# Kernel tuning notes

Measured on AMD Instinct MI355X. Metric: run time of the kernel, lower is better.

## Reference

```python
import jax, jax.numpy as jnp
import numpy as np

THRESHOLD = 1.25
CURRENT_DECAY = 0.25
VOLTAGE_DECAY = 0.03
SPIKE_PROB = 0.2


def setup_inputs() -> dict:
    key = jax.random.key(0)
    k1, k2 = jax.random.split(key)
    B, N, T = 2048, 16, 1024
    # binary input spike trains [batch, neurons, time]
    spike = (jax.random.uniform(k1, (B, N, T)) < SPIKE_PROB).astype(jnp.float32)
    # Dense synapse weight [out, in], no bias (lava-dl Dense default)
    W = jax.random.normal(k2, (N, N), dtype=jnp.float32) / np.sqrt(N)
    return {"spike": spike, "W": W}


def _cuba_dense(spike, W):
    # synaptic current input per timestep: z[b,o,t]
    z = jnp.einsum('oi,bit->bot', W, spike)
    zt = jnp.moveaxis(z, -1, 0)  # [T, B, O] for scan over time

    def step(carry, x):
        c, v = carry
        c = c * (1.0 - CURRENT_DECAY) + x
        v = v * (1.0 - VOLTAGE_DECAY) + c
        s = (v >= THRESHOLD).astype(v.dtype)
        v = v * (1.0 - s)  # hard reset to zero on spike
        return (c, v), s

    zero = jnp.zeros_like(zt[0])
    _, s = jax.lax.scan(step, (zero, zero), zt)  # s: [T, B, O]
    return jnp.moveaxis(s, 0, -1)  # [B, O, T]


def reference(spike, W):
    y = _cuba_dense(spike, W)  # [B, O, T] binary spikes
    # log-cosh free energy: exp(sum_neurons log(2 cosh(y))) -> [B, T]
    return jnp.exp(jnp.sum(jnp.log(2.0 * jnp.cosh(y)), axis=1))
```

## Files before the change

### kernel.cpp

```cpp
#include <hip/hip_runtime.h>
#include <stdint.h>

#define T_STEPS 1024
#define NWORDS  256
#define NB      8
#define SCAN_BLOCK (NB * 16)

typedef float f32x4 __attribute__((ext_vector_type(4)));

__global__ __launch_bounds__(256) void k_maskify(const float* __restrict__ spike,
                                                 unsigned long long* __restrict__ masks) {
    const int b  = blockIdx.x;
    const int tc = threadIdx.x;
    const float4* sp = reinterpret_cast<const float4*>(spike) + (size_t)b * (16 * NWORDS);
    unsigned int m0 = 0, m1 = 0, m2 = 0, m3 = 0;
#pragma unroll
    for (int i = 0; i < 16; ++i) {
        float4 v = sp[i * NWORDS + tc];
        m0 |= (v.x >= 0.5f) ? (1u << i) : 0u;
        m1 |= (v.y >= 0.5f) ? (1u << i) : 0u;
        m2 |= (v.z >= 0.5f) ? (1u << i) : 0u;
        m3 |= (v.w >= 0.5f) ? (1u << i) : 0u;
    }
    masks[(size_t)b * NWORDS + tc] =
        (unsigned long long)m0 | ((unsigned long long)m1 << 16) |
        ((unsigned long long)m2 << 32) | ((unsigned long long)m3 << 48);
}

__global__ __launch_bounds__(SCAN_BLOCK, 1) void k_scan(const float* __restrict__ W,
                                                        const unsigned long long* __restrict__ masks,
                                                        float* __restrict__ out) {
    __shared__ double ztab8[2][256][17];
    __shared__ unsigned long long mlds[NB][NWORDS + 1];

    const int tid = threadIdx.x;
    const int bb  = tid >> 4;
    const int o   = tid & 15;
    const int b   = blockIdx.x * NB + bb;

    {
        double w[16];
#pragma unroll
        for (int j = 0; j < 16; ++j) w[j] = (double)W[o * 16 + j];
#pragma unroll
        for (int k = 0; k < 64; ++k) {
            const int e    = tid + k * SCAN_BLOCK;
            const int byte = (e >> 4) & 255;
            const int s    = k >> 5;
            double slo = 0.0, shi = 0.0;
#pragma unroll
            for (int j = 0; j < 4; ++j) slo += (byte & (1 << j))  ? w[8 * s + j]     : 0.0;
#pragma unroll
            for (int j = 0; j < 4; ++j) shi += (byte & (16 << j)) ? w[8 * s + 4 + j] : 0.0;
            ztab8[s][byte][o] = slo + shi;
        }
    }
    {
        const unsigned long long* src = masks + (size_t)blockIdx.x * NB * NWORDS;
        for (int e = tid; e < NB * NWORDS; e += SCAN_BLOCK)
            mlds[e >> 8][e & 255] = src[e];
    }
    __syncthreads();

    const uint32_t tl0 = (uint32_t)(uintptr_t)(&ztab8[0][0][0]) + (uint32_t)(o * 8);
    const uint32_t tl1 = (uint32_t)(uintptr_t)(&ztab8[1][0][0]) + (uint32_t)(o * 8);
    const uint32_t mlb = (uint32_t)(uintptr_t)(&mlds[bb][0]);

    const uint64_t ob_out = (uint64_t)out;
    const uint32_t vb_out = (uint32_t)(b * (T_STEPS * 4));
    const int grp_sh      = tid & 48;
    const bool writer     = (o == 0);

    double c = 0.0, v = 0.0;

    double TA_0, TA_1, TA_2, TA_3, TA_4, TA_5, TA_6, TA_7;
    double TB_0, TB_1, TB_2, TB_3, TB_4, TB_5, TB_6, TB_7;
    unsigned long long MA, MB, MC, MD, q0, q1;

#define DSR(DST, ADDR) asm volatile("ds_read_b64 %0, %1" : "=v"(DST) : "v"(ADDR))
#define DSRM(DST, IDX) do { int _mi = (IDX); if (_mi > 255) _mi = 255;                \
    const uint32_t _a = mlb + ((uint32_t)_mi << 3); DSR(DST, _a); } while (0)
#define WAITLG(N) asm volatile("s_waitcnt lgkmcnt(" #N ")" ::: "memory")
#define WAITV(N)  asm volatile("s_waitcnt vmcnt(" #N ")" ::: "memory")
#define SBAR __builtin_amdgcn_sched_barrier(0)

#define TISSUE(P, MW) do {                                                            \
    const uint32_t _lo = (uint32_t)(MW), _hi = (uint32_t)((MW) >> 32);                \
    uint32_t _a;                                                                      \
    _a = tl0 + (_lo & 255u) * 136u;         DSR(P##_0, _a);                           \
    _a = tl1 + ((_lo >> 8) & 255u) * 136u;  DSR(P##_1, _a);                           \
    _a = tl0 + ((_lo >> 16) & 255u) * 136u; DSR(P##_2, _a);                           \
    _a = tl1 + (_lo >> 24) * 136u;          DSR(P##_3, _a);                           \
    _a = tl0 + (_hi & 255u) * 136u;         DSR(P##_4, _a);                           \
    _a = tl1 + ((_hi >> 8) & 255u) * 136u;  DSR(P##_5, _a);                           \
    _a = tl0 + ((_hi >> 16) & 255u) * 136u; DSR(P##_6, _a);                           \
    _a = tl1 + (_hi >> 24) * 136u;          DSR(P##_7, _a);                           \
} while (0)

#define ZSTEP(ZL, ZH, OWEL) do {                                                      \
    const double _z = (ZL) + (ZH);                                                    \
    c = fma(c, 0.75, _z);                                                             \
    v = fma(v, 0.97, c);                                                              \
    const bool _s = (v >= 1.25);                                                      \
    const unsigned long long _bal = __ballot(_s);                                     \
    v = _s ? 0.0 : v;                                                                 \
    const uint32_t _k = __popc((uint32_t)(_bal >> grp_sh) & 0xFFFFu);                 \
    OWEL = exp2f(fmaf((float)_k, 0.62581400f, 16.0f));                                \
} while (0)

#define COMPUTE(P, WD) do {                                                           \
    f32x4 _ow;                                                                        \
    ZSTEP(P##_0, P##_1, _ow.x);                                                       \
    ZSTEP(P##_2, P##_3, _ow.y);                                                       \
    ZSTEP(P##_4, P##_5, _ow.z);                                                       \
    ZSTEP(P##_6, P##_7, _ow.w);                                                       \
    if (writer) {                                                                     \
        const uint32_t _vo = vb_out + ((uint32_t)(WD) << 4);                          \
        asm volatile("global_store_dwordx4 %0, %1, %2"                                \
                     :: "v"(_vo), "v"(_ow), "s"(ob_out) : "memory");                  \
    }                                                                                 \
} while (0)

#define BODY(WD, P, MU, MI) do {                                                      \
    WAITLG(9); WAITV(16); SBAR;           \
    COMPUTE(P, WD);                                                                   \
    TISSUE(P, MU);                            \
    DSRM(MI, (WD) + 4); SBAR;                                                         \
} while (0)

    asm volatile("s_waitcnt vmcnt(0) lgkmcnt(0)" ::: "memory");

    DSRM(q0, 0); DSRM(q1, 1);
    WAITLG(0); SBAR;
    TISSUE(TA, q0); DSRM(MA, 2);
    TISSUE(TB, q1); DSRM(MB, 3); SBAR;

    for (int w = 0; w < 252; w += 4) {
        BODY(w,     TA, MA, MC);
        BODY(w + 1, TB, MB, MD);
        BODY(w + 2, TA, MC, MA);
        BODY(w + 3, TB, MD, MB);
    }
    BODY(252, TA, MA, MC);
    BODY(253, TB, MB, MD);

    WAITLG(9); SBAR;
    COMPUTE(TA, 254);
    WAITLG(0); SBAR;
    COMPUTE(TB, 255);
    asm volatile("s_waitcnt vmcnt(0)" ::: "memory");

#undef DSR
#undef DSRM
#undef WAITLG
#undef WAITV
#undef SBAR
#undef TISSUE
#undef ZSTEP
#undef COMPUTE
#undef BODY
}

__global__ __launch_bounds__(SCAN_BLOCK) void k_scan_fb(const float* __restrict__ W,
                                                        const float* __restrict__ spike,
                                                        float* __restrict__ out) {
    __shared__ double ztab[4][16][16];
    __shared__ unsigned long long mlds[NB][NWORDS];
    __shared__ float outtab[17];
    const int tid = threadIdx.x, bb = tid >> 4, o = tid & 15;
    for (int e = tid; e < 4 * 16 * 16; e += SCAN_BLOCK) {
        const int oo = e & 15, idx = (e >> 4) & 15, seg = e >> 8;
        double s = 0.0;
#pragma unroll
        for (int j = 0; j < 4; ++j)
            if (idx & (1 << j)) s += (double)W[oo * 16 + seg * 4 + j];
        ztab[seg][idx][oo] = s;
    }
    if (tid < 17) {
        const double ln2 = 0.69314718055994530941723212145818;
        const double l2c1 = log(2.0 * cosh(1.0));
        outtab[tid] = (float)exp((16.0 - (double)tid) * ln2 + (double)tid * l2c1);
    }
    {
        const int part = tid & 15;
        const float4* spb = reinterpret_cast<const float4*>(spike) +
                            (size_t)(blockIdx.x * NB + bb) * (16 * NWORDS);
        for (int w = 0; w < 16; ++w) {
            const int tc = part * 16 + w;
            unsigned int m0 = 0, m1 = 0, m2 = 0, m3 = 0;
#pragma unroll
            for (int i = 0; i < 16; ++i) {
                float4 v = spb[i * NWORDS + tc];
                m0 |= (v.x >= 0.5f) ? (1u << i) : 0u;
                m1 |= (v.y >= 0.5f) ? (1u << i) : 0u;
                m2 |= (v.z >= 0.5f) ? (1u << i) : 0u;
                m3 |= (v.w >= 0.5f) ? (1u << i) : 0u;
            }
            mlds[bb][tc] = (unsigned long long)m0 | ((unsigned long long)m1 << 16) |
                           ((unsigned long long)m2 << 32) | ((unsigned long long)m3 << 48);
        }
    }
    __syncthreads();
    double c = 0.0, v = 0.0;
    const int b = blockIdx.x * NB + bb;
    float* outp = out + (size_t)b * T_STEPS;
    const int grp_sh = tid & 48;
    const bool writer = (o == 0);
    for (int tg = 0; tg < NWORDS; ++tg) {
        const unsigned long long mw = mlds[bb][tg];
#pragma unroll
        for (int j = 0; j < 4; ++j) {
            const unsigned int m = (unsigned int)(mw >> (16 * j)) & 0xFFFFu;
            const double z = (ztab[0][m & 15][o] + ztab[1][(m >> 4) & 15][o]) +
                             (ztab[2][(m >> 8) & 15][o] + ztab[3][(m >> 12) & 15][o]);
            c = fma(c, 0.75, z);
            v = fma(v, 0.97, c);
            const bool s = (v >= 1.25);
            const unsigned long long bal = __ballot(s);
            v = s ? 0.0 : v;
            if (writer) outp[tg * 4 + j] = outtab[(int)__popcll((bal >> grp_sh) & 0xFFFFull)];
        }
    }
}

extern "C" void kernel_launch(void* const* d_in, const int* in_sizes, int n_in,
                              void* d_out, int out_size, void* d_ws, size_t ws_size,
                              hipStream_t stream) {
    const float* spike = (const float*)d_in[0];
    const float* W     = (const float*)d_in[1];
    float* out         = (float*)d_out;

    const int B = in_sizes[0] / (16 * T_STEPS);

    const size_t mask_bytes = (size_t)B * NWORDS * sizeof(unsigned long long);

    if (ws_size >= mask_bytes) {
        unsigned long long* masks = (unsigned long long*)d_ws;
        k_maskify<<<B, 256, 0, stream>>>(spike, masks);
        k_scan<<<B / NB, SCAN_BLOCK, 0, stream>>>(W, masks, out);
    } else {
        k_scan_fb<<<B / NB, SCAN_BLOCK, 0, stream>>>(W, spike, out);
    }
}
```

Before: 95.61 us.

## Interleave two independent batch recurrences per thread in a single-wave scan block

The scan kernel now uses one 64-thread wave per block. Each thread advances two independent batch rows (b and b+4) in lockstep, so their serial FMA, ballot and compare chains can interleave and hide each other's latency. The previous double-buffered lookup prefetch across iterations is replaced by a full LDS wait each step, so less memory latency is hidden ahead of compute. The number of blocks is unchanged but each block now has half as many threads, which lowers per-CU wave concurrency.

```diff
diff --git a/kernel.cpp b/kernel.cpp
--- a/kernel.cpp
+++ b/kernel.cpp
@@ -3,8 +3,7 @@
 
 #define T_STEPS 1024
 #define NWORDS  256
-#define NB      8
-#define SCAN_BLOCK (NB * 16)
+#define SCAN_BLOCK 64
 
 typedef float f32x4 __attribute__((ext_vector_type(4)));
 
@@ -31,22 +30,23 @@
                                                         const unsigned long long* __restrict__ masks,
                                                         float* __restrict__ out) {
     __shared__ double ztab8[2][256][17];
-    __shared__ unsigned long long mlds[NB][NWORDS + 1];
+    __shared__ unsigned long long mlds[8][NWORDS + 1];
 
     const int tid = threadIdx.x;
     const int bb  = tid >> 4;
     const int o   = tid & 15;
-    const int b   = blockIdx.x * NB + bb;
+    const int bx  = blockIdx.x * 8 + bb;
+    const int by  = bx + 4;
 
     {
         double w[16];
 #pragma unroll
         for (int j = 0; j < 16; ++j) w[j] = (double)W[o * 16 + j];
 #pragma unroll
-        for (int k = 0; k < 64; ++k) {
+        for (int k = 0; k < 128; ++k) {
             const int e    = tid + k * SCAN_BLOCK;
             const int byte = (e >> 4) & 255;
-            const int s    = k >> 5;
+            const int s    = k >> 6;
             double slo = 0.0, shi = 0.0;
 #pragma unroll
             for (int j = 0; j < 4; ++j) slo += (byte & (1 << j))  ? w[8 * s + j]     : 0.0;
@@ -56,30 +56,33 @@
         }
     }
     {
-        const unsigned long long* src = masks + (size_t)blockIdx.x * NB * NWORDS;
-        for (int e = tid; e < NB * NWORDS; e += SCAN_BLOCK)
+        const unsigned long long* src = masks + (size_t)blockIdx.x * 8 * NWORDS;
+        for (int e = tid; e < 8 * NWORDS; e += SCAN_BLOCK)
             mlds[e >> 8][e & 255] = src[e];
     }
     __syncthreads();
 
-    const uint32_t tl0 = (uint32_t)(uintptr_t)(&ztab8[0][0][0]) + (uint32_t)(o * 8);
-    const uint32_t tl1 = (uint32_t)(uintptr_t)(&ztab8[1][0][0]) + (uint32_t)(o * 8);
-    const uint32_t mlb = (uint32_t)(uintptr_t)(&mlds[bb][0]);
+    const uint32_t tl0  = (uint32_t)(uintptr_t)(&ztab8[0][0][0]) + (uint32_t)(o * 8);
+    const uint32_t tl1  = (uint32_t)(uintptr_t)(&ztab8[1][0][0]) + (uint32_t)(o * 8);
+    const uint32_t mlbx = (uint32_t)(uintptr_t)(&mlds[bb][0]);
+    const uint32_t mlby = (uint32_t)(uintptr_t)(&mlds[bb + 4][0]);
 
     const uint64_t ob_out = (uint64_t)out;
-    const uint32_t vb_out = (uint32_t)(b * (T_STEPS * 4));
+    const uint32_t vb_ox  = (uint32_t)(bx * (T_STEPS * 4));
+    const uint32_t vb_oy  = (uint32_t)(by * (T_STEPS * 4));
     const int grp_sh      = tid & 48;
     const bool writer     = (o == 0);
 
-    double c = 0.0, v = 0.0;
-
-    double TA_0, TA_1, TA_2, TA_3, TA_4, TA_5, TA_6, TA_7;
-    double TB_0, TB_1, TB_2, TB_3, TB_4, TB_5, TB_6, TB_7;
-    unsigned long long MA, MB, MC, MD, q0, q1;
+    double cx = 0.0, vx = 0.0, cy = 0.0, vy = 0.0;
+    float px0, px1, px2, px3, py0, py1, py2, py3;
+
+    double TAx_0, TAx_1, TAx_2, TAx_3, TAx_4, TAx_5, TAx_6, TAx_7;
+    double TAy_0, TAy_1, TAy_2, TAy_3, TAy_4, TAy_5, TAy_6, TAy_7;
+    unsigned long long MXa, MYa, MXb, MYb;
 
 #define DSR(DST, ADDR) asm volatile("ds_read_b64 %0, %1" : "=v"(DST) : "v"(ADDR))
-#define DSRM(DST, IDX) do { int _mi = (IDX); if (_mi > 255) _mi = 255;                \
-    const uint32_t _a = mlb + ((uint32_t)_mi << 3); DSR(DST, _a); } while (0)
+#define DSRM(DST, IDX, MLB) do { int _mi = (IDX); if (_mi > 255) _mi = 255;           \
+    const uint32_t _a = (MLB) + ((uint32_t)_mi << 3); DSR(DST, _a); } while (0)
 #define WAITLG(N) asm volatile("s_waitcnt lgkmcnt(" #N ")" ::: "memory")
 #define WAITV(N)  asm volatile("s_waitcnt vmcnt(" #N ")" ::: "memory")
 #define SBAR __builtin_amdgcn_sched_barrier(0)
@@ -97,57 +100,51 @@
     _a = tl1 + (_hi >> 24) * 136u;          DSR(P##_7, _a);                           \
 } while (0)
 
-#define ZSTEP(ZL, ZH, OWEL) do {                                                      \
+#define ZSTEP(CC, VV, ZL, ZH, OWEL) do {                                              \
     const double _z = (ZL) + (ZH);                                                    \
-    c = fma(c, 0.75, _z);                                                             \
-    v = fma(v, 0.97, c);                                                              \
-    const bool _s = (v >= 1.25);                                                      \
+    CC = fma(CC, 0.75, _z);                                                           \
+    VV = fma(VV, 0.97, CC);                                                           \
+    const bool _s = (VV >= 1.25);                                                     \
     const unsigned long long _bal = __ballot(_s);                                     \
-    v = _s ? 0.0 : v;                                                                 \
+    VV = _s ? 0.0 : VV;                                                               \
     const uint32_t _k = __popc((uint32_t)(_bal >> grp_sh) & 0xFFFFu);                 \
     OWEL = exp2f(fmaf((float)_k, 0.62581400f, 16.0f));                                \
 } while (0)
 
-#define COMPUTE(P, WD) do {                                                           \
-    f32x4 _ow;                                                                        \
-    ZSTEP(P##_0, P##_1, _ow.x);                                                       \
-    ZSTEP(P##_2, P##_3, _ow.y);                                                       \
-    ZSTEP(P##_4, P##_5, _ow.z);                                                       \
-    ZSTEP(P##_6, P##_7, _ow.w);                                                       \
+#define STOREW(WD, VB, O0, O1, O2, O3) do {                                           \
     if (writer) {                                                                     \
-        const uint32_t _vo = vb_out + ((uint32_t)(WD) << 4);                          \
+        f32x4 _ow; _ow.x = O0; _ow.y = O1; _ow.z = O2; _ow.w = O3;                    \
+        const uint32_t _vo = (VB) + ((uint32_t)(WD) << 4);                            \
         asm volatile("global_store_dwordx4 %0, %1, %2"                                \
                      :: "v"(_vo), "v"(_ow), "s"(ob_out) : "memory");                  \
     }                                                                                 \
 } while (0)
 
-#define BODY(WD, P, MU, MI) do {                                                      \
-    WAITLG(9); WAITV(16); SBAR;           \
-    COMPUTE(P, WD);                                                                   \
-    TISSUE(P, MU);                            \
-    DSRM(MI, (WD) + 4); SBAR;                                                         \
+#define BODY(WD, MUX, MUY, MLX, MLY) do {                                             \
+    WAITLG(0); SBAR;                        \
+    TISSUE(TAx, MUX);                                                                 \
+    TISSUE(TAy, MUY);                                                                 \
+    DSRM(MLX, (WD) + 1, mlbx);                                                        \
+    DSRM(MLY, (WD) + 1, mlby);                                                        \
+    WAITLG(2); SBAR;                        \
+    ZSTEP(cx, vx, TAx_0, TAx_1, px0); ZSTEP(cy, vy, TAy_0, TAy_1, py0);               \
+    ZSTEP(cx, vx, TAx_2, TAx_3, px1); ZSTEP(cy, vy, TAy_2, TAy_3, py1);               \
+    ZSTEP(cx, vx, TAx_4, TAx_5, px2); ZSTEP(cy, vy, TAy_4, TAy_5, py2);               \
+    ZSTEP(cx, vx, TAx_6, TAx_7, px3); ZSTEP(cy, vy, TAy_6, TAy_7, py3);               \
+    STOREW(WD, vb_ox, px0, px1, px2, px3);                                            \
+    STOREW(WD, vb_oy, py0, py1, py2, py3);                                            \
+    WAITV(16);                                        \
 } while (0)
 
     asm volatile("s_waitcnt vmcnt(0) lgkmcnt(0)" ::: "memory");
 
-    DSRM(q0, 0); DSRM(q1, 1);
-    WAITLG(0); SBAR;
-    TISSUE(TA, q0); DSRM(MA, 2);
-    TISSUE(TB, q1); DSRM(MB, 3); SBAR;
-
-    for (int w = 0; w < 252; w += 4) {
-        BODY(w,     TA, MA, MC);
-        BODY(w + 1, TB, MB, MD);
-        BODY(w + 2, TA, MC, MA);
-        BODY(w + 3, TB, MD, MB);
-    }
-    BODY(252, TA, MA, MC);
-    BODY(253, TB, MB, MD);
-
-    WAITLG(9); SBAR;
-    COMPUTE(TA, 254);
-    WAITLG(0); SBAR;
-    COMPUTE(TB, 255);
+    DSRM(MXa, 0, mlbx); DSRM(MYa, 0, mlby);
+
+    for (int w = 0; w < 256; w += 2) {
+        BODY(w,     MXa, MYa, MXb, MYb);
+        BODY(w + 1, MXb, MYb, MXa, MYa);
+    }
+
     asm volatile("s_waitcnt vmcnt(0)" ::: "memory");
 
 #undef DSR
@@ -157,18 +154,18 @@
 #undef SBAR
 #undef TISSUE
 #undef ZSTEP
-#undef COMPUTE
+#undef STOREW
 #undef BODY
 }
 
-__global__ __launch_bounds__(SCAN_BLOCK) void k_scan_fb(const float* __restrict__ W,
-                                                        const float* __restrict__ spike,
-                                                        float* __restrict__ out) {
+__global__ __launch_bounds__(128) void k_scan_fb(const float* __restrict__ W,
+                                                 const float* __restrict__ spike,
+                                                 float* __restrict__ out) {
     __shared__ double ztab[4][16][16];
-    __shared__ unsigned long long mlds[NB][NWORDS];
+    __shared__ unsigned long long mlds[8][NWORDS];
     __shared__ float outtab[17];
     const int tid = threadIdx.x, bb = tid >> 4, o = tid & 15;
-    for (int e = tid; e < 4 * 16 * 16; e += SCAN_BLOCK) {
+    for (int e = tid; e < 4 * 16 * 16; e += 128) {
         const int oo = e & 15, idx = (e >> 4) & 15, seg = e >> 8;
         double s = 0.0;
 #pragma unroll
@@ -184,7 +181,7 @@
     {
         const int part = tid & 15;
         const float4* spb = reinterpret_cast<const float4*>(spike) +
-                            (size_t)(blockIdx.x * NB + bb) * (16 * NWORDS);
+                            (size_t)(blockIdx.x * 8 + bb) * (16 * NWORDS);
         for (int w = 0; w < 16; ++w) {
             const int tc = part * 16 + w;
             unsigned int m0 = 0, m1 = 0, m2 = 0, m3 = 0;
@@ -202,7 +199,7 @@
     }
     __syncthreads();
     double c = 0.0, v = 0.0;
-    const int b = blockIdx.x * NB + bb;
+    const int b = blockIdx.x * 8 + bb;
     float* outp = out + (size_t)b * T_STEPS;
     const int grp_sh = tid & 48;
     const bool writer = (o == 0);
@@ -237,8 +234,8 @@
     if (ws_size >= mask_bytes) {
         unsigned long long* masks = (unsigned long long*)d_ws;
         k_maskify<<<B, 256, 0, stream>>>(spike, masks);
-        k_scan<<<B / NB, SCAN_BLOCK, 0, stream>>>(W, masks, out);
+        k_scan<<<B / 8, SCAN_BLOCK, 0, stream>>>(W, masks, out);
     } else {
-        k_scan_fb<<<B / NB, SCAN_BLOCK, 0, stream>>>(W, spike, out);
-    }
-}
+        k_scan_fb<<<B / 8, 128, 0, stream>>>(W, spike, out);
+    }
+}
```

Measured after the change: 158.8 us. 1.66x slower.
